# Optimization experiments

Hardware: AMD Instinct MI355X
Metric: run time of the kernel (lower is better)

## Reference

```python
import jax, jax.numpy as jnp
import numpy as np

N, D, M, E, K = 16384, 512, 1024, 8, 2
LOSS_COEF = 0.01
EPS = 1e-10


def setup_inputs() -> dict:
    key = jax.random.key(0)
    ks = jax.random.split(key, 6)
    x = jax.random.normal(ks[0], (N, D), dtype=jnp.float32)
    # gate weight (torch init is zeros; use small random so routing is non-degenerate)
    w_gate = 0.02 * jax.random.normal(ks[1], (D, E), dtype=jnp.float32)
    # stacked expert FFN params: Linear(D->M), GELU, Linear(M->D)
    W1 = jax.random.normal(ks[2], (E, D, M), dtype=jnp.float32) / np.sqrt(D)
    b1 = jnp.zeros((E, M), dtype=jnp.float32)
    W2 = jax.random.normal(ks[3], (E, M, D), dtype=jnp.float32) / np.sqrt(M)
    b2 = jnp.zeros((E, D), dtype=jnp.float32)
    return {"x": x, "w_gate": w_gate, "W1": W1, "b1": b1, "W2": W2, "b2": b2}


def _cv_squared(v):
    # torch .var() is unbiased (ddof=1)
    v = v.astype(jnp.float32)
    return jnp.var(v, ddof=1) / (jnp.mean(v) ** 2 + EPS)


def reference(x, w_gate, W1, b1, W2, b2):
    n = x.shape[0]
    # --- noisy_top_k_gating (eval path: no noise) ---
    logits = x @ w_gate                                  # [N, E]
    top_logits, top_idx = jax.lax.top_k(logits, min(K + 1, E))
    topk_logits = top_logits[:, :K]                      # [N, K]
    topk_idx = top_idx[:, :K]                            # [N, K]
    topk_gates = jax.nn.softmax(topk_logits, axis=-1)    # [N, K]
    gates = jnp.zeros_like(logits).at[jnp.arange(n)[:, None], topk_idx].set(topk_gates)
    importance = gates.sum(axis=0)                       # [E]
    load = (gates > 0).sum(axis=0).astype(jnp.float32)   # [E]
    loss = LOSS_COEF * (_cv_squared(importance) + _cv_squared(load))
    # --- experts (dense equivalent of sparse dispatch/combine: gate==0 rows contribute 0) ---
    h = jnp.einsum('nd,edm->enm', x, W1) + b1[:, None, :]     # [E, N, M]
    h = jax.nn.gelu(h, approximate=False)
    out = jnp.einsum('enm,emd->end', h, W2) + b2[:, None, :]  # [E, N, D]
    y = jnp.einsum('ne,end->nd', gates, out)                  # [N, D]
    return (y, loss)
```

## Files before the change

kernel.cpp:

```cpp
#include <hip/hip_runtime.h>
#include <math.h>

#define NTOK 16384
#define DDIM 512
#define MDIM 1024
#define NEXP 8
#define LDSW 32
#define TMAX 264

typedef __attribute__((ext_vector_type(8))) short short8;
typedef __attribute__((ext_vector_type(4))) float floatx4;

__device__ inline unsigned short f2bf(float f){
  union { float f; unsigned int u; } v; v.f = f;
  unsigned int u = v.u;
  u += ((u >> 16) & 1u) + 0x7fffu;
  return (unsigned short)(u >> 16);
}

__device__ inline float bf2f(unsigned short s){
  union { unsigned int u; float f; } v;
  v.u = ((unsigned int)s) << 16;
  return v.f;
}

__device__ inline float gelu_fast(float x){
  float u = x * 0.70710678118654752f;
  float a = fabsf(u);
  float t = __builtin_amdgcn_rcpf(fmaf(0.3275911f, a, 1.0f));
  float p = fmaf(1.061405429f, t, -1.453152027f);
  p = fmaf(p, t, 1.421413741f);
  p = fmaf(p, t, -0.284496736f);
  p = fmaf(p, t, 0.254829592f);
  p = p * t;
  float e = __expf(-u * u);
  float erfa = fmaf(-p, e, 1.0f);
  float erfu = copysignf(erfa, u);
  return 0.5f * x * (1.0f + erfu);
}

__device__ __forceinline__ void gload16(const unsigned short* g, unsigned short* l){
  __builtin_amdgcn_global_load_lds(
      (const __attribute__((address_space(1))) void*)g,
      (__attribute__((address_space(3))) void*)l,
      16, 0, 0);
}


__global__ void init_small_kernel(int* counts, float* imp){
  int t = threadIdx.x;
  if (t < NEXP){ counts[t] = 0; imp[t] = 0.0f; }
}

__global__ void transpose_conv_kernel(const float* __restrict__ in,
                                      unsigned short* __restrict__ out,
                                      int R, int C){
  __shared__ float tile[32][33];
  int e  = blockIdx.z;
  int c0 = blockIdx.x << 5;
  int r0 = blockIdx.y << 5;
  const float* src = in + (size_t)e * R * C;
  unsigned short* dst = out + (size_t)e * R * C;
  int tc = threadIdx.x;
  int tr = threadIdx.y;
  #pragma unroll
  for (int i = 0; i < 32; i += 8)
    tile[tr + i][tc] = src[(size_t)(r0 + tr + i) * C + c0 + tc];
  __syncthreads();
  #pragma unroll
  for (int i = 0; i < 32; i += 8)
    dst[(size_t)(c0 + tr + i) * R + r0 + tc] = f2bf(tile[tc][tr + i]);
}


__global__ __launch_bounds__(256)
void gating_kernel(const float* __restrict__ x,
                   const float* __restrict__ wg,
                   unsigned short* __restrict__ xb,
                   int* __restrict__ tok_e, float* __restrict__ tok_g,
                   int* __restrict__ counts, float* __restrict__ imp){
  __shared__ int   lcnt[NEXP];
  __shared__ float limp[NEXP];
  int t = threadIdx.x;
  if (t < NEXP){ lcnt[t] = 0; limp[t] = 0.0f; }
  __syncthreads();

  int wave = t >> 6;
  int lane = t & 63;

  for (int it = 0; it < 16; it++){
    int n = blockIdx.x * 64 + it * 4 + wave;

    const float4* xp = (const float4*)(x + (size_t)n * DDIM + lane * 8);
    float4 a = xp[0], b = xp[1];
    float xv[8] = {a.x, a.y, a.z, a.w, b.x, b.y, b.z, b.w};

    short8 xo;
    #pragma unroll
    for (int j = 0; j < 8; j++) xo[j] = (short)f2bf(xv[j]);
    *(short8*)(xb + (size_t)n * DDIM + lane * 8) = xo;

    double acc[NEXP];
    #pragma unroll
    for (int e = 0; e < NEXP; e++) acc[e] = 0.0;
    #pragma unroll
    for (int j = 0; j < 8; j++){
      const float* wr = wg + (size_t)(lane * 8 + j) * NEXP;
      #pragma unroll
      for (int e = 0; e < NEXP; e++) acc[e] += (double)xv[j] * (double)wr[e];
    }
    #pragma unroll
    for (int off = 32; off >= 1; off >>= 1){
      #pragma unroll
      for (int e = 0; e < NEXP; e++) acc[e] += __shfl_xor(acc[e], off);
    }
    if (lane == 0){
      int i0 = -1, i1 = -1;
      double l0 = -1e300, l1 = -1e300;
      #pragma unroll
      for (int e = 0; e < NEXP; e++){
        double v = acc[e];
        if (v > l0){ l1 = l0; i1 = i0; l0 = v; i0 = e; }
        else if (v > l1){ l1 = v; i1 = e; }
      }
      float ex = expf((float)(l1 - l0));
      float g0 = 1.0f / (1.0f + ex);
      float g1 = ex / (1.0f + ex);
      tok_e[n * 2]     = i0; tok_e[n * 2 + 1] = i1;
      tok_g[n * 2]     = g0; tok_g[n * 2 + 1] = g1;
      atomicAdd(&lcnt[i0], 1); atomicAdd(&lcnt[i1], 1);
      atomicAdd(&limp[i0], g0); atomicAdd(&limp[i1], g1);
    }
  }
  __syncthreads();
  if (t < NEXP){
    atomicAdd(&counts[t], lcnt[t]);
    atomicAdd(&imp[t], limp[t]);
  }
}

__global__ void loss_scan_kernel(const int* __restrict__ counts,
                                 const float* __restrict__ imp,
                                 int* __restrict__ offsets, int* __restrict__ cursor,
                                 int* __restrict__ tile_pre,
                                 float* __restrict__ out_loss){
  int off = 0, tp = 0;
  double si = 0, si2 = 0, sl = 0, sl2 = 0;
  for (int e = 0; e < NEXP; e++){
    offsets[e] = off; cursor[e] = off;
    tile_pre[e] = tp;
    tp += (counts[e] + 127) >> 7;
    off += counts[e];
    double im = (double)imp[e];
    double ld = (double)counts[e];
    si += im; si2 += im * im;
    sl += ld; sl2 += ld * ld;
  }
  offsets[NEXP] = off;
  tile_pre[NEXP] = tp;
  double mi = si / 8.0, ml = sl / 8.0;
  double vi = (si2 - 8.0 * mi * mi) / 7.0;
  double vl = (sl2 - 8.0 * ml * ml) / 7.0;
  double loss = 0.01 * (vi / (mi * mi + 1e-10) + vl / (ml * ml + 1e-10));
  *out_loss = (float)loss;
}

__global__ __launch_bounds__(256)
void scatter_kernel(const int* __restrict__ tok_e,
                    int* __restrict__ cursor,
                    int* __restrict__ btok, int* __restrict__ slot_of){
  __shared__ int lcnt[NEXP];
  __shared__ int lbase[NEXP];
  int t = threadIdx.x;
  if (t < NEXP) lcnt[t] = 0;
  __syncthreads();

  int n = blockIdx.x * 256 + t;
  int e0 = tok_e[n * 2], e1 = tok_e[n * 2 + 1];
  int r0 = atomicAdd(&lcnt[e0], 1);
  int r1 = atomicAdd(&lcnt[e1], 1);
  __syncthreads();
  if (t < NEXP) lbase[t] = atomicAdd(&cursor[t], lcnt[t]);
  __syncthreads();
  int s0 = lbase[e0] + r0;
  int s1 = lbase[e1] + r1;
  btok[s0] = n;
  btok[s1] = n;
  slot_of[n * 2]     = s0;
  slot_of[n * 2 + 1] = s1;
}


__global__ __launch_bounds__(256)
void gemm1_kernel(const unsigned short* __restrict__ xb,
                  const unsigned short* __restrict__ w1t,
                  const float* __restrict__ b1,
                  const int* __restrict__ offsets,
                  const int* __restrict__ tile_pre,
                  const int* __restrict__ btok,
                  unsigned short* __restrict__ H){
  int ct = blockIdx.x / TMAX;
  int tt = blockIdx.x % TMAX;
  if (tt >= tile_pre[NEXP]) return;
  int e = 0;
  while (tt >= tile_pre[e + 1]) e++;
  int rt = tt - tile_pre[e];
  int off = offsets[e];
  int cnt = offsets[e + 1] - off;
  int r0 = rt << 7;

  __shared__ unsigned short As[128 * LDSW];
  __shared__ unsigned short Bs[128 * LDSW];

  int t = threadIdx.x;
  int srow = t >> 2;
  int scol = (t & 3) << 3;
  int w = t >> 6;

  int ra0 = r0 + srow;        if (ra0 >= cnt) ra0 = cnt - 1;
  int ra1 = r0 + 64 + srow;   if (ra1 >= cnt) ra1 = cnt - 1;
  const unsigned short* aptr0 = xb + (size_t)btok[off + ra0] * DDIM + scol;
  const unsigned short* aptr1 = xb + (size_t)btok[off + ra1] * DDIM + scol;
  const unsigned short* bptr0 = w1t + ((size_t)e * MDIM + (ct << 7) + srow) * DDIM + scol;
  const unsigned short* bptr1 = bptr0 + (size_t)64 * DDIM;

  unsigned short* As0 = As + w * 512;
  unsigned short* As1 = As + 2048 + w * 512;
  unsigned short* Bs0 = Bs + w * 512;
  unsigned short* Bs1 = Bs + 2048 + w * 512;

  int lane = t & 63;
  int wr = (w >> 1) << 6;
  int wc = (w & 1) << 6;
  int lm = lane & 15;
  int lq = lane >> 4;

  const unsigned short* Ar[4];
  const unsigned short* Br[4];
  #pragma unroll
  for (int i = 0; i < 4; i++){
    Ar[i] = &As[(wr + i * 16 + lm) * LDSW + lq * 8];
    Br[i] = &Bs[(wc + i * 16 + lm) * LDSW + lq * 8];
  }

  floatx4 acc[4][4] = {};
  for (int k0 = 0; k0 < DDIM; k0 += 32){
    gload16(aptr0 + k0, As0);
    gload16(aptr1 + k0, As1);
    gload16(bptr0 + k0, Bs0);
    gload16(bptr1 + k0, Bs1);
    __syncthreads();
    short8 af[4], bf[4];
    #pragma unroll
    for (int i = 0; i < 4; i++) af[i] = *(const short8*)Ar[i];
    #pragma unroll
    for (int j = 0; j < 4; j++) bf[j] = *(const short8*)Br[j];
    #pragma unroll
    for (int i = 0; i < 4; i++)
      #pragma unroll
      for (int j = 0; j < 4; j++)
        acc[i][j] = __builtin_amdgcn_mfma_f32_16x16x32_bf16(af[i], bf[j], acc[i][j], 0, 0, 0);
    __syncthreads();
  }

  const float* bias = b1 + e * MDIM + (ct << 7);
  #pragma unroll
  for (int i = 0; i < 4; i++){
    int rbase = wr + i * 16 + lq * 4;
    #pragma unroll
    for (int j = 0; j < 4; j++){
      int cc = wc + j * 16 + lm;
      float bv = bias[cc];
      #pragma unroll
      for (int r = 0; r < 4; r++){
        int row = r0 + rbase + r;
        if (row < cnt){
          float v = acc[i][j][r] + bv;
          H[(size_t)(off + row) * MDIM + (ct << 7) + cc] = f2bf(gelu_fast(v));
        }
      }
    }
  }
}

__global__ __launch_bounds__(256)
void gemm2_kernel(const unsigned short* __restrict__ H,
                  const unsigned short* __restrict__ w2t,
                  const float* __restrict__ b2,
                  const int* __restrict__ offsets,
                  const int* __restrict__ tile_pre,
                  unsigned short* __restrict__ O){
  int ct = blockIdx.x / TMAX;
  int tt = blockIdx.x % TMAX;
  if (tt >= tile_pre[NEXP]) return;
  int e = 0;
  while (tt >= tile_pre[e + 1]) e++;
  int rt = tt - tile_pre[e];
  int off = offsets[e];
  int cnt = offsets[e + 1] - off;
  int r0 = rt << 7;

  __shared__ unsigned short As[128 * LDSW];
  __shared__ unsigned short Bs[128 * LDSW];

  int t = threadIdx.x;
  int srow = t >> 2;
  int scol = (t & 3) << 3;
  int w = t >> 6;

  int ra0 = r0 + srow;        if (ra0 >= cnt) ra0 = cnt - 1;
  int ra1 = r0 + 64 + srow;   if (ra1 >= cnt) ra1 = cnt - 1;
  const unsigned short* aptr0 = H + (size_t)(off + ra0) * MDIM + scol;
  const unsigned short* aptr1 = H + (size_t)(off + ra1) * MDIM + scol;
  const unsigned short* bptr0 = w2t + ((size_t)e * DDIM + (ct << 7) + srow) * MDIM + scol;
  const unsigned short* bptr1 = bptr0 + (size_t)64 * MDIM;

  unsigned short* As0 = As + w * 512;
  unsigned short* As1 = As + 2048 + w * 512;
  unsigned short* Bs0 = Bs + w * 512;
  unsigned short* Bs1 = Bs + 2048 + w * 512;

  int lane = t & 63;
  int wr = (w >> 1) << 6;
  int wc = (w & 1) << 6;
  int lm = lane & 15;
  int lq = lane >> 4;

  const unsigned short* Ar[4];
  const unsigned short* Br[4];
  #pragma unroll
  for (int i = 0; i < 4; i++){
    Ar[i] = &As[(wr + i * 16 + lm) * LDSW + lq * 8];
    Br[i] = &Bs[(wc + i * 16 + lm) * LDSW + lq * 8];
  }

  floatx4 acc[4][4] = {};
  for (int k0 = 0; k0 < MDIM; k0 += 32){
    gload16(aptr0 + k0, As0);
    gload16(aptr1 + k0, As1);
    gload16(bptr0 + k0, Bs0);
    gload16(bptr1 + k0, Bs1);
    __syncthreads();
    short8 af[4], bf[4];
    #pragma unroll
    for (int i = 0; i < 4; i++) af[i] = *(const short8*)Ar[i];
    #pragma unroll
    for (int j = 0; j < 4; j++) bf[j] = *(const short8*)Br[j];
    #pragma unroll
    for (int i = 0; i < 4; i++)
      #pragma unroll
      for (int j = 0; j < 4; j++)
        acc[i][j] = __builtin_amdgcn_mfma_f32_16x16x32_bf16(af[i], bf[j], acc[i][j], 0, 0, 0);
    __syncthreads();
  }

  const float* bias = b2 + e * DDIM + (ct << 7);
  #pragma unroll
  for (int i = 0; i < 4; i++){
    int rbase = wr + i * 16 + lq * 4;
    #pragma unroll
    for (int j = 0; j < 4; j++){
      int cc = wc + j * 16 + lm;
      float bv = bias[cc];
      #pragma unroll
      for (int r = 0; r < 4; r++){
        int row = r0 + rbase + r;
        if (row < cnt)
          O[(size_t)(off + row) * DDIM + (ct << 7) + cc] = f2bf(acc[i][j][r] + bv);
      }
    }
  }
}


__global__ __launch_bounds__(256)
void combine_kernel(const unsigned short* __restrict__ O,
                    const float* __restrict__ tok_g,
                    const int* __restrict__ slot_of,
                    float* __restrict__ y){
  int wave = threadIdx.x >> 6;
  int lane = threadIdx.x & 63;
  int n = blockIdx.x * 4 + wave;
  int s0 = slot_of[n * 2], s1 = slot_of[n * 2 + 1];
  float g0 = tok_g[n * 2], g1 = tok_g[n * 2 + 1];
  short8 a = *(const short8*)(O + (size_t)s0 * DDIM + lane * 8);
  short8 b = *(const short8*)(O + (size_t)s1 * DDIM + lane * 8);
  float4 o0, o1;
  float* po0 = (float*)&o0;
  float* po1 = (float*)&o1;
  #pragma unroll
  for (int j = 0; j < 4; j++){
    po0[j] = g0 * bf2f((unsigned short)a[j]) + g1 * bf2f((unsigned short)b[j]);
    po1[j] = g0 * bf2f((unsigned short)a[j + 4]) + g1 * bf2f((unsigned short)b[j + 4]);
  }
  float4* yp = (float4*)(y + (size_t)n * DDIM + lane * 8);
  yp[0] = o0;
  yp[1] = o1;
}


extern "C" void kernel_launch(void* const* d_in, const int* in_sizes, int n_in,
                              void* d_out, int out_size, void* d_ws, size_t ws_size,
                              hipStream_t stream){
  const float* x  = (const float*)d_in[0];
  const float* wg = (const float*)d_in[1];
  const float* W1 = (const float*)d_in[2];
  const float* b1 = (const float*)d_in[3];
  const float* W2 = (const float*)d_in[4];
  const float* b2 = (const float*)d_in[5];
  float* y = (float*)d_out;

  char* ws = (char*)d_ws;
  size_t o = 0;
  auto alloc = [&](size_t bytes)->char*{
    char* p = ws + o;
    o += (bytes + 255) & ~(size_t)255;
    return p;
  };
  unsigned short* xb   = (unsigned short*)alloc((size_t)NTOK * DDIM * 2);
  unsigned short* w1t  = (unsigned short*)alloc((size_t)NEXP * MDIM * DDIM * 2);
  unsigned short* w2t  = (unsigned short*)alloc((size_t)NEXP * DDIM * MDIM * 2);
  unsigned short* H    = (unsigned short*)alloc((size_t)NTOK * 2 * MDIM * 2);
  unsigned short* O    = (unsigned short*)alloc((size_t)NTOK * 2 * DDIM * 2);
  int*   btok    = (int*)  alloc((size_t)NTOK * 2 * 4);
  int*   slot_of = (int*)  alloc((size_t)NTOK * 2 * 4);
  int*   tok_e   = (int*)  alloc((size_t)NTOK * 2 * 4);
  float* tok_g   = (float*)alloc((size_t)NTOK * 2 * 4);
  int*   counts  = (int*)  alloc(64);
  float* imp     = (float*)alloc(64);
  int*   offsets = (int*)  alloc(64);
  int*   cursor  = (int*)  alloc(64);
  int*   tile_pre= (int*)  alloc(64);

  hipLaunchKernelGGL(init_small_kernel, dim3(1), dim3(64), 0, stream, counts, imp);
  hipLaunchKernelGGL(transpose_conv_kernel, dim3(MDIM / 32, DDIM / 32, NEXP), dim3(32, 8), 0, stream,
                     W1, w1t, DDIM, MDIM);
  hipLaunchKernelGGL(transpose_conv_kernel, dim3(DDIM / 32, MDIM / 32, NEXP), dim3(32, 8), 0, stream,
                     W2, w2t, MDIM, DDIM);
  hipLaunchKernelGGL(gating_kernel, dim3(NTOK / 64), dim3(256), 0, stream,
                     x, wg, xb, tok_e, tok_g, counts, imp);
  hipLaunchKernelGGL(loss_scan_kernel, dim3(1), dim3(1), 0, stream,
                     counts, imp, offsets, cursor, tile_pre, y + (size_t)NTOK * DDIM);
  hipLaunchKernelGGL(scatter_kernel, dim3(NTOK / 256), dim3(256), 0, stream,
                     tok_e, cursor, btok, slot_of);
  hipLaunchKernelGGL(gemm1_kernel, dim3(TMAX * 8), dim3(256), 0, stream,
                     xb, w1t, b1, offsets, tile_pre, btok, H);
  hipLaunchKernelGGL(gemm2_kernel, dim3(TMAX * 4), dim3(256), 0, stream,
                     H, w2t, b2, offsets, tile_pre, O);
  hipLaunchKernelGGL(combine_kernel, dim3(NTOK / 4), dim3(256), 0, stream,
                     O, tok_g, slot_of, y);
}
```

Before: 305.6 us.

## Double-buffer LDS in expert GEMMs, swizzle block order, widen gating grid

Both expert GEMM kernels now use two LDS buffers, so loads for the next K-slice (async gload16) are issued while MFMAs run on the current slice. This halves the barriers per K step and hides global-load latency, at the cost of doubled shared memory per block. Block indices are remapped so that consecutive blocks share the same row tile across column tiles, which should improve L2 reuse of the A operand and spread work over the XCDs. The gating kernel now runs four times as many blocks, each handling fewer tokens, to raise parallelism.

```diff
diff --git a/kernel.cpp b/kernel.cpp
--- a/kernel.cpp
+++ b/kernel.cpp
@@ -88,8 +88,8 @@
   int wave = t >> 6;
   int lane = t & 63;
 
-  for (int it = 0; it < 16; it++){
-    int n = blockIdx.x * 64 + it * 4 + wave;
+  for (int it = 0; it < 4; it++){
+    int n = blockIdx.x * 16 + it * 4 + wave;
 
     const float4* xp = (const float4*)(x + (size_t)n * DDIM + lane * 8);
     float4 a = xp[0], b = xp[1];
@@ -191,6 +191,30 @@
 }
 
 
+__device__ __forceinline__ void stage_step(const unsigned short* aptr0, const unsigned short* aptr1,
+                                           const unsigned short* bptr0, const unsigned short* bptr1,
+                                           int k0, unsigned short* Ab, unsigned short* Bb, int wbase){
+  gload16(aptr0 + k0, Ab + wbase);
+  gload16(aptr1 + k0, Ab + 2048 + wbase);
+  gload16(bptr0 + k0, Bb + wbase);
+  gload16(bptr1 + k0, Bb + 2048 + wbase);
+}
+
+__device__ __forceinline__ void mfma_step(const unsigned short* A, const unsigned short* B,
+                                          const int* aoff, const int* boff,
+                                          floatx4 acc[4][4]){
+  short8 af[4], bfrag[4];
+  #pragma unroll
+  for (int i = 0; i < 4; i++) af[i] = *(const short8*)(A + aoff[i]);
+  #pragma unroll
+  for (int j = 0; j < 4; j++) bfrag[j] = *(const short8*)(B + boff[j]);
+  #pragma unroll
+  for (int i = 0; i < 4; i++)
+    #pragma unroll
+    for (int j = 0; j < 4; j++)
+      acc[i][j] = __builtin_amdgcn_mfma_f32_16x16x32_bf16(af[i], bfrag[j], acc[i][j], 0, 0, 0);
+}
+
 __global__ __launch_bounds__(256)
 void gemm1_kernel(const unsigned short* __restrict__ xb,
                   const unsigned short* __restrict__ w1t,
@@ -199,8 +223,10 @@
                   const int* __restrict__ tile_pre,
                   const int* __restrict__ btok,
                   unsigned short* __restrict__ H){
-  int ct = blockIdx.x / TMAX;
-  int tt = blockIdx.x % TMAX;
+  int b = blockIdx.x;
+  int L = (b & 7) * TMAX + (b >> 3);
+  int ct = L & 7;
+  int tt = L >> 3;
   if (tt >= tile_pre[NEXP]) return;
   int e = 0;
   while (tt >= tile_pre[e + 1]) e++;
@@ -209,8 +235,8 @@
   int cnt = offsets[e + 1] - off;
   int r0 = rt << 7;
 
-  __shared__ unsigned short As[128 * LDSW];
-  __shared__ unsigned short Bs[128 * LDSW];
+  __shared__ unsigned short As[2][128 * LDSW];
+  __shared__ unsigned short Bs[2][128 * LDSW];
 
   int t = threadIdx.x;
   int srow = t >> 2;
@@ -224,10 +250,7 @@
   const unsigned short* bptr0 = w1t + ((size_t)e * MDIM + (ct << 7) + srow) * DDIM + scol;
   const unsigned short* bptr1 = bptr0 + (size_t)64 * DDIM;
 
-  unsigned short* As0 = As + w * 512;
-  unsigned short* As1 = As + 2048 + w * 512;
-  unsigned short* Bs0 = Bs + w * 512;
-  unsigned short* Bs1 = Bs + 2048 + w * 512;
+  int wbase = w * 512;
 
   int lane = t & 63;
   int wr = (w >> 1) << 6;
@@ -235,31 +258,25 @@
   int lm = lane & 15;
   int lq = lane >> 4;
 
-  const unsigned short* Ar[4];
-  const unsigned short* Br[4];
+  int aoff[4], boff[4];
   #pragma unroll
   for (int i = 0; i < 4; i++){
-    Ar[i] = &As[(wr + i * 16 + lm) * LDSW + lq * 8];
-    Br[i] = &Bs[(wc + i * 16 + lm) * LDSW + lq * 8];
+    aoff[i] = (wr + i * 16 + lm) * LDSW + lq * 8;
+    boff[i] = (wc + i * 16 + lm) * LDSW + lq * 8;
   }
 
   floatx4 acc[4][4] = {};
-  for (int k0 = 0; k0 < DDIM; k0 += 32){
-    gload16(aptr0 + k0, As0);
-    gload16(aptr1 + k0, As1);
-    gload16(bptr0 + k0, Bs0);
-    gload16(bptr1 + k0, Bs1);
+
+  stage_step(aptr0, aptr1, bptr0, bptr1, 0, As[0], Bs[0], wbase);
+  __syncthreads();
+  for (int k0 = 0; k0 < DDIM; k0 += 64){
+    if (k0 + 32 < DDIM)
+      stage_step(aptr0, aptr1, bptr0, bptr1, k0 + 32, As[1], Bs[1], wbase);
+    mfma_step(As[0], Bs[0], aoff, boff, acc);
     __syncthreads();
-    short8 af[4], bf[4];
-    #pragma unroll
-    for (int i = 0; i < 4; i++) af[i] = *(const short8*)Ar[i];
-    #pragma unroll
-    for (int j = 0; j < 4; j++) bf[j] = *(const short8*)Br[j];
-    #pragma unroll
-    for (int i = 0; i < 4; i++)
-      #pragma unroll
-      for (int j = 0; j < 4; j++)
-        acc[i][j] = __builtin_amdgcn_mfma_f32_16x16x32_bf16(af[i], bf[j], acc[i][j], 0, 0, 0);
+    if (k0 + 64 < DDIM)
+      stage_step(aptr0, aptr1, bptr0, bptr1, k0 + 64, As[0], Bs[0], wbase);
+    mfma_step(As[1], Bs[1], aoff, boff, acc);
     __syncthreads();
   }
 
@@ -290,8 +307,10 @@
                   const int* __restrict__ offsets,
                   const int* __restrict__ tile_pre,
                   unsigned short* __restrict__ O){
-  int ct = blockIdx.x / TMAX;
-  int tt = blockIdx.x % TMAX;
+  int b = blockIdx.x;
+  int L = (b & 7) * (TMAX / 2) + (b >> 3);
+  int ct = L & 3;
+  int tt = L >> 2;
   if (tt >= tile_pre[NEXP]) return;
   int e = 0;
   while (tt >= tile_pre[e + 1]) e++;
@@ -300,8 +319,8 @@
   int cnt = offsets[e + 1] - off;
   int r0 = rt << 7;
 
-  __shared__ unsigned short As[128 * LDSW];
-  __shared__ unsigned short Bs[128 * LDSW];
+  __shared__ unsigned short As[2][128 * LDSW];
+  __shared__ unsigned short Bs[2][128 * LDSW];
 
   int t = threadIdx.x;
   int srow = t >> 2;
@@ -315,10 +334,7 @@
   const unsigned short* bptr0 = w2t + ((size_t)e * DDIM + (ct << 7) + srow) * MDIM + scol;
   const unsigned short* bptr1 = bptr0 + (size_t)64 * MDIM;
 
-  unsigned short* As0 = As + w * 512;
-  unsigned short* As1 = As + 2048 + w * 512;
-  unsigned short* Bs0 = Bs + w * 512;
-  unsigned short* Bs1 = Bs + 2048 + w * 512;
+  int wbase = w * 512;
 
   int lane = t & 63;
   int wr = (w >> 1) << 6;
@@ -326,31 +342,25 @@
   int lm = lane & 15;
   int lq = lane >> 4;
 
-  const unsigned short* Ar[4];
-  const unsigned short* Br[4];
+  int aoff[4], boff[4];
   #pragma unroll
   for (int i = 0; i < 4; i++){
-    Ar[i] = &As[(wr + i * 16 + lm) * LDSW + lq * 8];
-    Br[i] = &Bs[(wc + i * 16 + lm) * LDSW + lq * 8];
+    aoff[i] = (wr + i * 16 + lm) * LDSW + lq * 8;
+    boff[i] = (wc + i * 16 + lm) * LDSW + lq * 8;
   }
 
   floatx4 acc[4][4] = {};
-  for (int k0 = 0; k0 < MDIM; k0 += 32){
-    gload16(aptr0 + k0, As0);
-    gload16(aptr1 + k0, As1);
-    gload16(bptr0 + k0, Bs0);
-    gload16(bptr1 + k0, Bs1);
+
+  stage_step(aptr0, aptr1, bptr0, bptr1, 0, As[0], Bs[0], wbase);
+  __syncthreads();
+  for (int k0 = 0; k0 < MDIM; k0 += 64){
+    if (k0 + 32 < MDIM)
+      stage_step(aptr0, aptr1, bptr0, bptr1, k0 + 32, As[1], Bs[1], wbase);
+    mfma_step(As[0], Bs[0], aoff, boff, acc);
     __syncthreads();
-    short8 af[4], bf[4];
-    #pragma unroll
-    for (int i = 0; i < 4; i++) af[i] = *(const short8*)Ar[i];
-    #pragma unroll
-    for (int j = 0; j < 4; j++) bf[j] = *(const short8*)Br[j];
-    #pragma unroll
-    for (int i = 0; i < 4; i++)
-      #pragma unroll
-      for (int j = 0; j < 4; j++)
-        acc[i][j] = __builtin_amdgcn_mfma_f32_16x16x32_bf16(af[i], bf[j], acc[i][j], 0, 0, 0);
+    if (k0 + 64 < MDIM)
+      stage_step(aptr0, aptr1, bptr0, bptr1, k0 + 64, As[0], Bs[0], wbase);
+    mfma_step(As[1], Bs[1], aoff, boff, acc);
     __syncthreads();
   }
 
@@ -437,7 +447,7 @@
                      W1, w1t, DDIM, MDIM);
   hipLaunchKernelGGL(transpose_conv_kernel, dim3(DDIM / 32, MDIM / 32, NEXP), dim3(32, 8), 0, stream,
                      W2, w2t, MDIM, DDIM);
-  hipLaunchKernelGGL(gating_kernel, dim3(NTOK / 64), dim3(256), 0, stream,
+  hipLaunchKernelGGL(gating_kernel, dim3(NTOK / 16), dim3(256), 0, stream,
                      x, wg, xb, tok_e, tok_g, counts, imp);
   hipLaunchKernelGGL(loss_scan_kernel, dim3(1), dim3(1), 0, stream,
                      counts, imp, offsets, cursor, tile_pre, y + (size_t)NTOK * DDIM);
```

After: 295.6 us. 1.03x faster.
